# Kernel tuning notes

Hardware: AMD Instinct MI355X
Metric: run time of the kernel (lower is better)

## Reference

```python
import jax, jax.numpy as jnp
import numpy as np

B = 65536      # total pedestrians
P = 16         # peds per scene (uniform segments)
S = B // P     # number of scenes
H = 128        # dec_h_dim
MLP = 256      # mlp_dim (enc_h_feat width)
Z = 32         # z_dim
T = 12         # seq_len
NS = 6         # n_state
NP = 2         # n_pred_state
ZX = MLP + Z


def setup_inputs() -> dict:
    key = jax.random.key(0)
    ks = jax.random.split(key, 24)
    n = lambda k, shp, s=1.0: (jax.random.normal(k, shp, jnp.float32) * s)
    w = 0.05  # weight scale
    starts = jnp.arange(S, dtype=jnp.int32) * P
    return {
        "last_state": n(ks[0], (B, NS)),
        "enc_h_feat": n(ks[1], (B, MLP)),
        "z": n(ks[2], (B, Z)),
        "seq_start_end": jnp.stack([starts, starts + P], axis=1),
        "fut_obst": jnp.zeros((T, B, 1), jnp.float32),  # unused by forward
        "fut_state": n(ks[3], (T, B, NP)),
        # dec_hidden: Linear(MLP+Z -> H)
        "W_dec": n(ks[4], (H, ZX), w), "b_dec": jnp.zeros((H,), jnp.float32),
        # to_vel: Linear(NS -> NP)
        "W_vel": n(ks[5], (NP, NS), w), "b_vel": jnp.zeros((NP,), jnp.float32),
        # GRUCell(input=ZX+NP, hidden=H): gate order r, z, n (PyTorch)
        "W_ih": n(ks[6], (3 * H, ZX + NP), w), "b_ih": jnp.zeros((3 * H,), jnp.float32),
        "W_hh": n(ks[7], (3 * H, H), w), "b_hh": jnp.zeros((3 * H,), jnp.float32),
        # fc_attn: Linear(2H -> H)
        "W_attn": n(ks[8], (H, 2 * H), w), "b_attn": jnp.zeros((H,), jnp.float32),
        # fc_mu / fc_std: Linear(H -> NP)
        "W_mu": n(ks[9], (NP, H), w), "b_mu": jnp.zeros((NP,), jnp.float32),
        "W_std": n(ks[10], (NP, H), w), "b_std": jnp.zeros((NP,), jnp.float32),
    }


def reference(last_state, enc_h_feat, z, seq_start_end, fut_obst, fut_state,
              W_dec, b_dec, W_vel, b_vel, W_ih, b_ih, W_hh, b_hh,
              W_attn, b_attn, W_mu, b_mu, W_std, b_std):
    zx = jnp.concatenate([enc_h_feat, z], axis=1)                 # [B, ZX]
    h0 = zx @ W_dec.T + b_dec                                     # [B, H]
    a0 = last_state @ W_vel.T + b_vel                             # [B, NP]

    # zx part of GRU input is constant across time -> precompute its gate contribution
    gx_zx = zx @ W_ih[:, :ZX].T + b_ih                            # [B, 3H]
    W_ia = W_ih[:, ZX:]                                           # [3H, NP]

    def step(carry, fut_t):
        h, a = carry
        gx = gx_zx + a @ W_ia.T                                   # input gates  [B, 3H]
        gh = h @ W_hh.T + b_hh                                    # hidden gates [B, 3H]
        rx, zxg, nx = jnp.split(gx, 3, axis=1)
        rh, zhg, nh = jnp.split(gh, 3, axis=1)
        r = jax.nn.sigmoid(rx + rh)
        zg = jax.nn.sigmoid(zxg + zhg)
        ng = jnp.tanh(nx + r * nh)
        h = (1.0 - zg) * ng + zg * h                              # GRUCell update

        # segment self-attention over uniform pedestrian segments
        hv = h.reshape(S, P, H)
        score = jnp.einsum('spd,sqd->spq', hv, hv)                # [S, P, P]
        attn = jax.nn.softmax(score, axis=-1)
        ctx = jnp.einsum('spq,sqd->spd', attn, hv).reshape(B, H)
        h = jnp.concatenate([h, ctx], axis=1) @ W_attn.T + b_attn # fc_attn

        mu = h @ W_mu.T + b_mu
        logvar = h @ W_std.T + b_std
        std = jnp.exp(0.5 * logvar)                               # sqrt(exp(logVar))
        return (h, fut_t), (mu, std)

    (_, _), (mus, stds) = jax.lax.scan(step, (h0, a0), fut_state)
    return mus, stds                                              # each [T, B, NP]
```

## Files before the change

kernel.cpp:

```cpp
#include <hip/hip_runtime.h>

#define B_TOT 65536
#define T_STEPS 12
#define LOG2E 1.44269504088896f

typedef short bf16x8 __attribute__((ext_vector_type(8)));
typedef float f32x4 __attribute__((ext_vector_type(4)));

__device__ __forceinline__ unsigned short f2b(float f) {
  unsigned u = __float_as_uint(f);
  u += 0x7fffu + ((u >> 16) & 1u);
  return (unsigned short)(u >> 16);
}
__device__ __forceinline__ float b2f(unsigned short s) {
  return __uint_as_float(((unsigned)s) << 16);
}
__device__ __forceinline__ float fexp2(float x) { return __builtin_amdgcn_exp2f(x); }
__device__ __forceinline__ float frcp(float x) { return __builtin_amdgcn_rcpf(x); }
__device__ __forceinline__ f32x4 mfma16(bf16x8 a, bf16x8 b, f32x4 c) {
  return __builtin_amdgcn_mfma_f32_16x16x32_bf16(a, b, c, 0, 0, 0);
}
__device__ __forceinline__ bf16x8 ld8(const unsigned short* p) {
  return *reinterpret_cast<const bf16x8*>(p);
}

__global__ void repack_weights(const float* __restrict__ Whh, const float* __restrict__ Wat,
                               const float* __restrict__ Wmu, const float* __restrict__ Wst,
                               unsigned short* __restrict__ ws) {
  int idx = blockIdx.x * 256 + threadIdx.x;
  if (idx < 49152) {
    int e = idx & 7, ln = (idx >> 3) & 63, kc = (idx >> 9) & 3, nt = idx >> 11;
    int rr = nt * 16 + (ln & 15), kk = kc * 32 + (ln >> 4) * 8 + e;
    ws[idx] = f2b(Whh[rr * 128 + kk]);
  } else if (idx < 81920) {
    int j = idx - 49152;
    int e = j & 7, ln = (j >> 3) & 63, kc = (j >> 9) & 7, nt = j >> 12;
    int rr = nt * 16 + (ln & 15), kk = kc * 32 + (ln >> 4) * 8 + e;
    ws[idx] = f2b(Wat[rr * 256 + kk]);
  } else if (idx < 83968) {
    int j = idx - 81920;
    int e = j & 7, ln = (j >> 3) & 63, kc = j >> 9;
    int rr = ln & 15, kk = kc * 32 + (ln >> 4) * 8 + e;
    float v = (rr < 2) ? Wmu[rr * 128 + kk] : ((rr < 4) ? Wst[(rr - 2) * 128 + kk] : 0.f);
    ws[idx] = f2b(v);
  }
}

__global__ __launch_bounds__(512, 4) void dec_main(
    const float* __restrict__ last_state, const float* __restrict__ enc,
    const float* __restrict__ zin, const float* __restrict__ fut,
    const float* __restrict__ Wdec, const float* __restrict__ bdec,
    const float* __restrict__ Wvel, const float* __restrict__ bvel,
    const float* __restrict__ Wih, const float* __restrict__ bih,
    const float* __restrict__ bhh, const float* __restrict__ batn,
    const float* __restrict__ bmu, const float* __restrict__ bstd,
    const unsigned short* __restrict__ fragW, float* __restrict__ out) {
  constexpr int HP = 136;
  constexpr int GXP = 388;
  constexpr int ZXP = 296;
  constexpr int HCP = 264;
  constexpr int TVP = 24;
  constexpr int HFP = 129;

  __shared__ __align__(16) unsigned short s_gxzx[32 * GXP];
  __shared__ __align__(16) unsigned short s_h[32 * HP];
  __shared__ __align__(16) float s_hf[32 * HFP];
  __shared__ __align__(16) unsigned short s_pool[14592];
  __shared__ __align__(16) unsigned short s_attn[2 * 16 * 16];
  __shared__ __align__(16) float s_a[32 * 2];

  const int tid = threadIdx.x;
  const int lane = tid & 63;
  const int wv = tid >> 6;
  const int c = lane & 15;
  const int rg = lane >> 4;
  const int row0 = blockIdx.x * 32;

  const bf16x8* fWhh = (const bf16x8*)(fragW);
  const bf16x8* fWat = (const bf16x8*)(fragW + 49152);
  const bf16x8* fWms = (const bf16x8*)(fragW + 81920);

  const int colR = wv * 16 + c;
  const float wr0 = Wih[(colR)*290 + 288], wr1 = Wih[(colR)*290 + 289];
  const float wz0 = Wih[(colR + 128) * 290 + 288], wz1 = Wih[(colR + 128) * 290 + 289];
  const float wn0 = Wih[(colR + 256) * 290 + 288], wn1 = Wih[(colR + 256) * 290 + 289];
  const float bhr = bhh[colR], bhz = bhh[colR + 128], bhn = bhh[colR + 256];
  const float ba = batn[colR];

#pragma unroll
  for (int i = 0; i < 4; ++i) {
    int f4 = tid + i * 512;
    int r = f4 >> 6, cc = (f4 & 63) << 2;
    const float4 v = *(const float4*)(enc + (size_t)(row0 + r) * 256 + cc);
    unsigned short* d = &s_pool[r * ZXP + cc];
    d[0] = f2b(v.x); d[1] = f2b(v.y); d[2] = f2b(v.z); d[3] = f2b(v.w);
  }
  if (tid < 256) {
    int r = tid >> 3, cc = (tid & 7) << 2;
    const float4 v = *(const float4*)(zin + (size_t)(row0 + r) * 32 + cc);
    unsigned short* d = &s_pool[r * ZXP + 256 + cc];
    d[0] = f2b(v.x); d[1] = f2b(v.y); d[2] = f2b(v.z); d[3] = f2b(v.w);
  }
  if (tid < 64) {
    int r = tid >> 1, j = tid & 1;
    float s = bvel[j];
#pragma unroll
    for (int k = 0; k < 6; ++k) s += last_state[(size_t)(row0 + r) * 6 + k] * Wvel[j * 6 + k];
    s_a[r * 2 + j] = s;
  }
  __syncthreads();

#pragma unroll 1
  for (int i = 0; i < 4; ++i) {
    const int nt = wv + 8 * i;
    const bool isH = (i == 3);
    const int nrow = isH ? colR : (nt * 16 + c);
    const float* wp = isH ? (Wdec + (size_t)nrow * 288) : (Wih + (size_t)nrow * 290);
    f32x4 acc[2] = {{0.f, 0.f, 0.f, 0.f}, {0.f, 0.f, 0.f, 0.f}};
#pragma unroll 1
    for (int kc = 0; kc < 9; ++kc) {
      const float* bp = wp + kc * 32 + rg * 8;
      bf16x8 Bf;
#pragma unroll
      for (int e = 0; e < 8; ++e) Bf[e] = (short)f2b(bp[e]);
#pragma unroll
      for (int m = 0; m < 2; ++m) {
        bf16x8 A = ld8(&s_pool[(m * 16 + c) * ZXP + kc * 32 + rg * 8]);
        acc[m] = mfma16(A, Bf, acc[m]);
      }
    }
    if (isH) {
      const float bias = bdec[colR];
#pragma unroll
      for (int m = 0; m < 2; ++m)
#pragma unroll
        for (int r4 = 0; r4 < 4; ++r4) {
          int row = m * 16 + rg * 4 + r4;
          float v = acc[m][r4] + bias;
          s_h[row * HP + colR] = f2b(v);
          s_hf[row * HFP + colR] = v;
        }
    } else {
      const float bias = bih[nt * 16 + c];
#pragma unroll
      for (int m = 0; m < 2; ++m)
#pragma unroll
        for (int r4 = 0; r4 < 4; ++r4) {
          int row = m * 16 + rg * 4 + r4;
          s_gxzx[row * GXP + nt * 16 + c] = f2b(acc[m][r4] + bias);
        }
    }
  }
  __syncthreads();

  unsigned short* s_hcat = s_pool;
  unsigned short* s_hvT = s_pool + 8448;
  const int sq = wv >> 2;
  const int q4 = wv & 3;

#pragma unroll 1
  for (int t = 0; t < T_STEPS; ++t) {
#pragma unroll 1
    for (int m = 0; m < 2; ++m) {
      f32x4 aR = {0.f, 0.f, 0.f, 0.f}, aZ = {0.f, 0.f, 0.f, 0.f}, aN = {0.f, 0.f, 0.f, 0.f};
#pragma unroll
      for (int kc = 0; kc < 4; ++kc) {
        bf16x8 A = ld8(&s_h[(m * 16 + c) * HP + kc * 32 + rg * 8]);
        aR = mfma16(A, fWhh[((wv)*4 + kc) * 64 + lane], aR);
        aZ = mfma16(A, fWhh[((wv + 8) * 4 + kc) * 64 + lane], aZ);
        aN = mfma16(A, fWhh[((wv + 16) * 4 + kc) * 64 + lane], aN);
      }
      const float4 aLo = *(const float4*)&s_a[(m * 16 + rg * 4) * 2];
      const float4 aHi = *(const float4*)&s_a[(m * 16 + rg * 4) * 2 + 4];
#pragma unroll
      for (int r4 = 0; r4 < 4; ++r4) {
        const int row = m * 16 + rg * 4 + r4;
        const float a0 = (r4 == 0) ? aLo.x : (r4 == 1) ? aLo.z : (r4 == 2) ? aHi.x : aHi.z;
        const float a1 = (r4 == 0) ? aLo.y : (r4 == 1) ? aLo.w : (r4 == 2) ? aHi.y : aHi.w;
        float gr = b2f(s_gxzx[row * GXP + colR]) + a0 * wr0 + a1 * wr1 + bhr + aR[r4];
        float gz = b2f(s_gxzx[row * GXP + 128 + colR]) + a0 * wz0 + a1 * wz1 + bhz + aZ[r4];
        float nx = b2f(s_gxzx[row * GXP + 256 + colR]) + a0 * wn0 + a1 * wn1;
        float nh = bhn + aN[r4];
        float rr = frcp(1.f + fexp2(-LOG2E * gr));
        float zz = frcp(1.f + fexp2(-LOG2E * gz));
        float xx = nx + rr * nh;
        xx = fminf(fmaxf(xx, -15.f), 15.f);
        float e2 = fexp2(2.f * LOG2E * xx);
        float nn = (e2 - 1.f) * frcp(e2 + 1.f);
        float hv = (1.f - zz) * nn + zz * s_hf[row * HFP + colR];
        unsigned short hb = f2b(hv);
        s_hcat[row * HCP + colR] = hb;
        s_hvT[(m * 128 + colR) * TVP + (row & 15)] = hb;
      }
    }
    __syncthreads();

    {
      f32x4 sc = {0.f, 0.f, 0.f, 0.f};
#pragma unroll
      for (int kc = 0; kc < 4; ++kc) {
        bf16x8 F = ld8(&s_hcat[(sq * 16 + c) * HCP + kc * 32 + rg * 8]);
        sc = mfma16(F, F, sc);
      }
      float v = (q4 == 0) ? sc[0] : (q4 == 1) ? sc[1] : (q4 == 2) ? sc[2] : sc[3];
      float mx = v;
#pragma unroll
      for (int d = 1; d < 16; d <<= 1) mx = fmaxf(mx, __shfl_xor(mx, d));
      float e = fexp2(LOG2E * (v - mx));
      float s = e;
#pragma unroll
      for (int d = 1; d < 16; d <<= 1) s += __shfl_xor(s, d);
      float p = e * frcp(s);
      s_attn[(sq * 16 + rg * 4 + q4) * 16 + c] = f2b(p);
    }
    __syncthreads();

    {
      bf16x8 Aat = {0, 0, 0, 0, 0, 0, 0, 0};
      if (lane < 32) Aat = ld8(&s_attn[(sq * 16 + c) * 16 + rg * 8]);
#pragma unroll
      for (int i = 0; i < 2; ++i) {
        const int dt = q4 * 2 + i;
        bf16x8 Bv = {0, 0, 0, 0, 0, 0, 0, 0};
        if (lane < 32) Bv = ld8(&s_hvT[(sq * 128 + dt * 16 + c) * TVP + rg * 8]);
        f32x4 zz4 = {0.f, 0.f, 0.f, 0.f};
        f32x4 cx = mfma16(Aat, Bv, zz4);
#pragma unroll
        for (int r4 = 0; r4 < 4; ++r4)
          s_hcat[(sq * 16 + rg * 4 + r4) * HCP + 128 + dt * 16 + c] = f2b(cx[r4]);
      }
      if (wv == 6 && t + 1 < T_STEPS)
        s_a[lane] = fut[(size_t)t * B_TOT * 2 + (size_t)row0 * 2 + lane];
    }
    __syncthreads();

#pragma unroll 1
    for (int m = 0; m < 2; ++m) {
      f32x4 acc = {0.f, 0.f, 0.f, 0.f};
#pragma unroll
      for (int kc = 0; kc < 8; ++kc) {
        bf16x8 A = ld8(&s_hcat[(m * 16 + c) * HCP + kc * 32 + rg * 8]);
        acc = mfma16(A, fWat[(wv * 8 + kc) * 64 + lane], acc);
      }
#pragma unroll
      for (int r4 = 0; r4 < 4; ++r4) {
        const int row = m * 16 + rg * 4 + r4;
        float v = acc[r4] + ba;
        s_h[row * HP + colR] = f2b(v);
        s_hf[row * HFP + colR] = v;
      }
    }
    __syncthreads();

    if (wv < 2) {
      f32x4 acc = {0.f, 0.f, 0.f, 0.f};
#pragma unroll
      for (int kc = 0; kc < 4; ++kc) {
        bf16x8 A = ld8(&s_h[(wv * 16 + c) * HP + kc * 32 + rg * 8]);
        acc = mfma16(A, fWms[kc * 64 + lane], acc);
      }
      if (c < 4) {
#pragma unroll
        for (int r4 = 0; r4 < 4; ++r4) {
          const int gb = row0 + wv * 16 + rg * 4 + r4;
          if (c < 2) {
            out[(size_t)t * B_TOT * 2 + (size_t)gb * 2 + c] = acc[r4] + bmu[c];
          } else {
            float lv = acc[r4] + bstd[c - 2];
            out[(size_t)T_STEPS * B_TOT * 2 + (size_t)t * B_TOT * 2 + (size_t)gb * 2 + (c - 2)] =
                fexp2(0.72134752044448f * lv);
          }
        }
      }
    }
  }
}

extern "C" void kernel_launch(void* const* d_in, const int* in_sizes, int n_in,
                              void* d_out, int out_size, void* d_ws, size_t ws_size,
                              hipStream_t stream) {
  const float* last_state = (const float*)d_in[0];
  const float* enc = (const float*)d_in[1];
  const float* zin = (const float*)d_in[2];
  const float* fut = (const float*)d_in[5];
  const float* Wdec = (const float*)d_in[6];
  const float* bdec = (const float*)d_in[7];
  const float* Wvel = (const float*)d_in[8];
  const float* bvel = (const float*)d_in[9];
  const float* Wih = (const float*)d_in[10];
  const float* bih = (const float*)d_in[11];
  const float* Whh = (const float*)d_in[12];
  const float* bhh = (const float*)d_in[13];
  const float* Wat = (const float*)d_in[14];
  const float* batn = (const float*)d_in[15];
  const float* Wmu = (const float*)d_in[16];
  const float* bmu = (const float*)d_in[17];
  const float* Wst = (const float*)d_in[18];
  const float* bstd = (const float*)d_in[19];

  unsigned short* ws = (unsigned short*)d_ws;
  repack_weights<<<328, 256, 0, stream>>>(Whh, Wat, Wmu, Wst, ws);
  dec_main<<<B_TOT / 32, 512, 0, stream>>>(last_state, enc, zin, fut, Wdec, bdec, Wvel, bvel,
                                           Wih, bih, bhh, batn, bmu, bstd, ws, (float*)d_out);
}
```

Baseline: 485.5 us.

## Fold mu/std heads into fc_attn weights and drop a per-step barrier

Precomputes combined weights W_mu·W_attn and W_std·W_attn, plus folded biases, in the repack kernel. The output heads can then be computed from the same hcat A-fragments inside the fc_attn MFMA loop by two waves, which removes a separate phase and one __syncthreads per timestep. The transposed h store is also packed into one 8-byte write, and the HFP padding is changed. This adds extra MFMAs and branching in two waves, and the folding changes where bf16 rounding happens.

```diff
diff --git a/kernel.cpp b/kernel.cpp
--- a/kernel.cpp
+++ b/kernel.cpp
@@ -26,7 +26,8 @@
 
 __global__ void repack_weights(const float* __restrict__ Whh, const float* __restrict__ Wat,
                                const float* __restrict__ Wmu, const float* __restrict__ Wst,
-                               unsigned short* __restrict__ ws) {
+                               const float* __restrict__ batn, const float* __restrict__ bmu,
+                               const float* __restrict__ bstd, unsigned short* __restrict__ ws) {
   int idx = blockIdx.x * 256 + threadIdx.x;
   if (idx < 49152) {
     int e = idx & 7, ln = (idx >> 3) & 63, kc = (idx >> 9) & 3, nt = idx >> 11;
@@ -37,12 +38,20 @@
     int e = j & 7, ln = (j >> 3) & 63, kc = (j >> 9) & 7, nt = j >> 12;
     int rr = nt * 16 + (ln & 15), kk = kc * 32 + (ln >> 4) * 8 + e;
     ws[idx] = f2b(Wat[rr * 256 + kk]);
-  } else if (idx < 83968) {
+  } else if (idx < 82944) {
     int j = idx - 81920;
-    int e = j & 7, ln = (j >> 3) & 63, kc = j >> 9;
-    int rr = ln & 15, kk = kc * 32 + (ln >> 4) * 8 + e;
-    float v = (rr < 2) ? Wmu[rr * 128 + kk] : ((rr < 4) ? Wst[(rr - 2) * 128 + kk] : 0.f);
-    ws[idx] = f2b(v);
+    int e = j & 7, rg = (j >> 3) & 3, cj = (j >> 5) & 3, kc = j >> 7;
+    int k = kc * 32 + rg * 8 + e;
+    const float* wrow = (cj < 2) ? (Wmu + cj * 128) : (Wst + (cj - 2) * 128);
+    float s = 0.f;
+    for (int d = 0; d < 128; ++d) s += wrow[d] * Wat[d * 256 + k];
+    ws[idx] = f2b(s);
+  } else if (idx < 82948) {
+    int cj = idx - 82944;
+    const float* wrow = (cj < 2) ? (Wmu + cj * 128) : (Wst + (cj - 2) * 128);
+    float s = (cj < 2) ? bmu[cj] : bstd[cj - 2];
+    for (int d = 0; d < 128; ++d) s += wrow[d] * batn[d];
+    ((float*)(ws + 82944))[cj] = s;
   }
 }
 
@@ -53,14 +62,13 @@
     const float* __restrict__ Wvel, const float* __restrict__ bvel,
     const float* __restrict__ Wih, const float* __restrict__ bih,
     const float* __restrict__ bhh, const float* __restrict__ batn,
-    const float* __restrict__ bmu, const float* __restrict__ bstd,
     const unsigned short* __restrict__ fragW, float* __restrict__ out) {
   constexpr int HP = 136;
   constexpr int GXP = 388;
   constexpr int ZXP = 296;
   constexpr int HCP = 264;
   constexpr int TVP = 24;
-  constexpr int HFP = 129;
+  constexpr int HFP = 130;
 
   __shared__ __align__(16) unsigned short s_gxzx[32 * GXP];
   __shared__ __align__(16) unsigned short s_h[32 * HP];
@@ -78,7 +86,8 @@
 
   const bf16x8* fWhh = (const bf16x8*)(fragW);
   const bf16x8* fWat = (const bf16x8*)(fragW + 49152);
-  const bf16x8* fWms = (const bf16x8*)(fragW + 81920);
+  const unsigned short* fWcb = fragW + 81920;
+  const float* bcb = (const float*)(fragW + 82944);
 
   const int colR = wv * 16 + c;
   const float wr0 = Wih[(colR)*290 + 288], wr1 = Wih[(colR)*290 + 289];
@@ -172,6 +181,7 @@
       }
       const float4 aLo = *(const float4*)&s_a[(m * 16 + rg * 4) * 2];
       const float4 aHi = *(const float4*)&s_a[(m * 16 + rg * 4) * 2 + 4];
+      f32x4 hv4;
 #pragma unroll
       for (int r4 = 0; r4 < 4; ++r4) {
         const int row = m * 16 + rg * 4 + r4;
@@ -188,10 +198,13 @@
         float e2 = fexp2(2.f * LOG2E * xx);
         float nn = (e2 - 1.f) * frcp(e2 + 1.f);
         float hv = (1.f - zz) * nn + zz * s_hf[row * HFP + colR];
-        unsigned short hb = f2b(hv);
-        s_hcat[row * HCP + colR] = hb;
-        s_hvT[(m * 128 + colR) * TVP + (row & 15)] = hb;
-      }
+        hv4[r4] = hv;
+        s_hcat[row * HCP + colR] = f2b(hv);
+      }
+      unsigned p01 = (unsigned)f2b(hv4[0]) | ((unsigned)f2b(hv4[1]) << 16);
+      unsigned p23 = (unsigned)f2b(hv4[2]) | ((unsigned)f2b(hv4[3]) << 16);
+      uint2 pk; pk.x = p01; pk.y = p23;
+      *(uint2*)&s_hvT[(m * 128 + colR) * TVP + rg * 4] = pk;
     }
     __syncthreads();
 
@@ -236,11 +249,18 @@
 
 #pragma unroll 1
     for (int m = 0; m < 2; ++m) {
+      const bool doOut = (wv == 0 && m == 0) || (wv == 4 && m == 1);
       f32x4 acc = {0.f, 0.f, 0.f, 0.f};
+      f32x4 acc2 = {0.f, 0.f, 0.f, 0.f};
 #pragma unroll
       for (int kc = 0; kc < 8; ++kc) {
         bf16x8 A = ld8(&s_hcat[(m * 16 + c) * HCP + kc * 32 + rg * 8]);
         acc = mfma16(A, fWat[(wv * 8 + kc) * 64 + lane], acc);
+        if (doOut) {
+          bf16x8 wf = {0, 0, 0, 0, 0, 0, 0, 0};
+          if (c < 4) wf = ld8(&fWcb[((kc * 4 + c) * 4 + rg) * 8]);
+          acc2 = mfma16(A, wf, acc2);
+        }
       }
 #pragma unroll
       for (int r4 = 0; r4 < 4; ++r4) {
@@ -249,30 +269,20 @@
         s_h[row * HP + colR] = f2b(v);
         s_hf[row * HFP + colR] = v;
       }
-    }
-    __syncthreads();
-
-    if (wv < 2) {
-      f32x4 acc = {0.f, 0.f, 0.f, 0.f};
-#pragma unroll
-      for (int kc = 0; kc < 4; ++kc) {
-        bf16x8 A = ld8(&s_h[(wv * 16 + c) * HP + kc * 32 + rg * 8]);
-        acc = mfma16(A, fWms[kc * 64 + lane], acc);
-      }
-      if (c < 4) {
+      if (doOut && c < 4) {
 #pragma unroll
         for (int r4 = 0; r4 < 4; ++r4) {
-          const int gb = row0 + wv * 16 + rg * 4 + r4;
+          const int gb = row0 + m * 16 + rg * 4 + r4;
           if (c < 2) {
-            out[(size_t)t * B_TOT * 2 + (size_t)gb * 2 + c] = acc[r4] + bmu[c];
+            out[(size_t)t * B_TOT * 2 + (size_t)gb * 2 + c] = acc2[r4] + bcb[c];
           } else {
-            float lv = acc[r4] + bstd[c - 2];
             out[(size_t)T_STEPS * B_TOT * 2 + (size_t)t * B_TOT * 2 + (size_t)gb * 2 + (c - 2)] =
-                fexp2(0.72134752044448f * lv);
+                fexp2(0.72134752044448f * (acc2[r4] + bcb[c]));
           }
         }
       }
     }
+    __syncthreads();
   }
 }
 
@@ -299,7 +309,7 @@
   const float* bstd = (const float*)d_in[19];
 
   unsigned short* ws = (unsigned short*)d_ws;
-  repack_weights<<<328, 256, 0, stream>>>(Whh, Wat, Wmu, Wst, ws);
+  repack_weights<<<328, 256, 0, stream>>>(Whh, Wat, Wmu, Wst, batn, bmu, bstd, ws);
   dec_main<<<B_TOT / 32, 512, 0, stream>>>(last_state, enc, zin, fut, Wdec, bdec, Wvel, bvel,
-                                           Wih, bih, bhh, batn, bmu, bstd, ws, (float*)d_out);
-}
+                                           Wih, bih, bhh, batn, ws, (float*)d_out);
+}
```

Measured after the change: 471.9 us. 2.8% less time.
